# Kernel tuning notes

Hardware: AMD Instinct MI355X
Metric: run time of the kernel (lower is better)

Reference implementation:

```python
import jax, jax.numpy as jnp
import numpy as np

C_IN, C = 16, 32
N = 150000
SHAPE = (480, 360, 32)
SLOPE = 0.01  # LeakyReLU default
EPS = 1e-5    # BatchNorm1d default

# offset index into the canonical 27-neighbor table, ordered (dz, dy, dx)
P133 = tuple(9 + (dy + 1) * 3 + (dx + 1) for dy in (-1, 0, 1) for dx in (-1, 0, 1))   # kernel (1,3,3)
P313 = tuple((dz + 1) * 9 + 3 + (dx + 1) for dz in (-1, 0, 1) for dx in (-1, 0, 1))   # kernel (3,1,3)
P311 = tuple((dz + 1) * 9 + 4 for dz in (-1, 0, 1))                                   # kernel (3,1,1)
P131 = tuple(9 + (dy + 1) * 3 + 1 for dy in (-1, 0, 1))                               # kernel (1,3,1)
P113 = (12, 13, 14)                                                                   # kernel (1,1,3)


def setup_inputs() -> dict:
    rng = np.random.default_rng(0)
    # unique active voxel linear coords, sorted for searchsorted lookup
    lin = np.sort(rng.choice(SHAPE[0] * SHAPE[1] * SHAPE[2], size=N, replace=False))
    z, yx = np.divmod(lin, SHAPE[1] * SHAPE[2])
    y, x = np.divmod(yx, SHAPE[2])
    coords = np.stack([z, y, x], 1)  # [N,3]
    offs = np.array([[dz, dy, dx] for dz in (-1, 0, 1) for dy in (-1, 0, 1) for dx in (-1, 0, 1)])
    nc = coords[None] + offs[:, None]  # [27,N,3]
    valid = (nc >= 0).all(-1) & (nc[..., 0] < SHAPE[0]) & (nc[..., 1] < SHAPE[1]) & (nc[..., 2] < SHAPE[2])
    nlin = nc[..., 0] * SHAPE[1] * SHAPE[2] + nc[..., 1] * SHAPE[2] + nc[..., 2]
    pos = np.clip(np.searchsorted(lin, nlin), 0, N - 1)
    found = valid & (lin[pos] == nlin)
    nbr = np.where(found, pos, -1).astype(np.int32)  # [27,N], spconv indice pairs

    key = jax.random.key(0)
    ks = jax.random.split(key, 9)
    w = lambda k, kk, ci, co: jax.random.normal(k, (kk, ci, co), jnp.float32) * (1.0 / np.sqrt(kk * ci))
    bn_params = jnp.stack([
        jnp.stack([1.0 + 0.1 * jax.random.normal(jax.random.fold_in(ks[8], 4 * i + 0), (C,)),
                   0.1 * jax.random.normal(jax.random.fold_in(ks[8], 4 * i + 1), (C,)),
                   0.1 * jax.random.normal(jax.random.fold_in(ks[8], 4 * i + 2), (C,)),
                   0.5 + jax.random.uniform(jax.random.fold_in(ks[8], 4 * i + 3), (C,))])
        for i in range(7)
    ])  # [7,4,C]: gamma, beta, running_mean, running_var
    return {
        "x_feat": jax.random.normal(ks[0], (N, C_IN), jnp.float32),
        "nbr": jnp.asarray(nbr),
        "W1": w(ks[1], 9, C_IN, C), "W12": w(ks[2], 9, C, C),
        "W2": w(ks[3], 9, C_IN, C), "W3": w(ks[4], 9, C, C),
        "Wr1": w(ks[5], 3, C, C), "Wr2": w(ks[6], 3, C, C), "Wr3": w(ks[7], 3, C, C),
        "bn_params": bn_params,
    }


def _subm(feat, nbr, W, offs):
    """Submanifold sparse conv: gather -> masked GEMM -> same active set."""
    idx = nbr[jnp.asarray(offs)]              # [K,N]
    g = feat[jnp.clip(idx, 0)]                # [K,N,Cin]
    g = jnp.where((idx >= 0)[..., None], g, jnp.zeros((), feat.dtype))
    return jnp.einsum('knc,kcd->nd', g, W)    # [N,Cout]


def _bn(f, p):  # eval-mode BatchNorm1d
    gamma, beta, mean, var = p[0], p[1], p[2], p[3]
    return gamma * (f - mean) * jax.lax.rsqrt(var + EPS) + beta


def _lrelu(f):
    return jnp.where(f >= 0, f, SLOPE * f)


def reference(x_feat, nbr, W1, W12, W2, W3, Wr1, Wr2, Wr3, bn_params):
    # ResContextBlock (downCntx): act then BN, per source
    s = _bn(_lrelu(_subm(x_feat, nbr, W1, P133)), bn_params[0])
    s = _bn(_lrelu(_subm(s, nbr, W12, P313)), bn_params[1])
    r = _bn(_lrelu(_subm(x_feat, nbr, W2, P313)), bn_params[2])
    r = _bn(_lrelu(_subm(r, nbr, W3, P133)), bn_params[3])
    y = r + s
    # ReconBlock: three axial convs -> BN -> sigmoid, summed, gating multiply
    a = jax.nn.sigmoid(_bn(_subm(y, nbr, Wr1, P311), bn_params[4]))
    b = jax.nn.sigmoid(_bn(_subm(y, nbr, Wr2, P131), bn_params[5]))
    c = jax.nn.sigmoid(_bn(_subm(y, nbr, Wr3, P113), bn_params[6]))
    return (a + b + c) * y
```

## Files before the change

kernel.cpp:

```cpp
#include <hip/hip_runtime.h>
#include <cstdint>
#include <cstddef>


#define SLOPE 0.01f
#define BN_EPS 1e-5f

typedef __attribute__((ext_vector_type(8))) short bf16x8;
typedef __attribute__((ext_vector_type(4))) float f32x4;

__device__ __forceinline__ float bflo(uint32_t w) {
    union { uint32_t i; float f; } v; v.i = w << 16; return v.f;
}
__device__ __forceinline__ float bfhi(uint32_t w) {
    union { uint32_t i; float f; } v; v.i = w & 0xffff0000u; return v.f;
}
__device__ __forceinline__ float bf2f(uint16_t u) {
    union { uint32_t i; float f; } v; v.i = ((uint32_t)u) << 16; return v.f;
}
__device__ __forceinline__ uint16_t f2bf(float f) {
    union { float f; uint32_t i; } v; v.f = f;
    uint32_t x = v.i;
    return (uint16_t)((x + 0x7fffu + ((x >> 16) & 1u)) >> 16);
}

struct Taps9 { int t[9]; };
struct WSrcs { const void* p[8]; };

#define WFS     18432
#define WF_END  (5 * WFS)
#define BN_CNT  896

__device__ __forceinline__ int detect_f32_inline(const uint16_t* x16)
{
    int lane = threadIdx.x & 63;
    float a = bf2f(x16[4 * lane]);
    float b = bf2f(x16[4 * lane + 2]);
    int bad = (!(a > -16.f && a < 16.f)) || (!(b > -16.f && b < 16.f));
    return __ballot(bad) != 0ull;
}

__device__ __forceinline__ float readw(const void* p, int j, int f32)
{
    return f32 ? ((const float*)p)[j] : bf2f(((const uint16_t*)p)[j]);
}

__global__ void prep_all(const uint16_t* __restrict__ xprobe, WSrcs srcs,
                         uint16_t* __restrict__ Wf, float* __restrict__ bnf)
{
    int f32 = detect_f32_inline(xprobe);
    int i = blockIdx.x * 256 + threadIdx.x;
    if (i < WF_END) {
        int s = i / WFS, r = i - s * WFS;
        int t = r >> 11, T = (r >> 10) & 1;
        int co = (r >> 5) & 31, k = r & 31;
        uint16_t outv;
        if (s == 0 || s == 2) {
            int c = k >> 1, p = k & 1;
            float w = readw(srcs.p[s == 0 ? 0 : 2], (t * 16 + c) * 32 + co, f32);
            uint16_t h = f2bf(w);
            outv = (T == 0) ? h : (p == 0 ? f2bf(w - bf2f(h)) : (uint16_t)0);
        } else {
            float w;
            if (s == 4) {
                int g = t / 3, kk = t - g * 3;
                const void* bnp = srcs.p[7];
                float ga = readw(bnp, (4 + g) * 128 + co, f32);
                float va = readw(bnp, (4 + g) * 128 + 96 + co, f32);
                float scl = ga * rsqrtf(va + BN_EPS);
                w = readw(srcs.p[4 + g], (kk * 32 + k) * 32 + co, f32) * scl;
            } else {
                w = readw(srcs.p[s == 1 ? 1 : 3], (t * 32 + k) * 32 + co, f32);
            }
            uint16_t h = f2bf(w);
            outv = (T == 0) ? h : f2bf(w - bf2f(h));
        }
        Wf[i] = outv;
    } else if (i < WF_END + BN_CNT) {
        bnf[i - WF_END] = readw(srcs.p[7], i - WF_END, f32);
    }
}

__global__ void canon_x3(const void* __restrict__ xsrc,
                         uint32_t* __restrict__ xi, int total)
{
    int f32 = detect_f32_inline((const uint16_t*)xsrc);
    for (int i = blockIdx.x * blockDim.x + threadIdx.x; i < total;
         i += gridDim.x * blockDim.x) {
        float v = f32 ? ((const float*)xsrc)[i]
                      : bf2f(((const uint16_t*)xsrc)[i]);
        int row = i >> 4, c = i & 15;
        uint16_t h = f2bf(v);
        uint16_t l = f2bf(v - bf2f(h));
        xi[(size_t)row * 16 + c] = (uint32_t)h | ((uint32_t)l << 16);
    }
}

struct ConvJob {
    const uint16_t* feat;
    const uint16_t* Wf;
    const float*    bn;
    const uint16_t* addsrc;
    uint16_t*       out;
    Taps9 taps;
};

#define MFMA_BF16(A, B, C) __builtin_amdgcn_mfma_f32_16x16x32_bf16(A, B, C, 0, 0, 0)

__launch_bounds__(256, 3)
__global__ void conv_mfma5(ConvJob j0, ConvJob j1,
                           const int* __restrict__ nbr, int N)
{
    const ConvJob J = (blockIdx.y == 1) ? j1 : j0;
    const int tid = threadIdx.x;
    const int n0  = blockIdx.x * 128;
    const int lane = tid & 63;
    const int m = lane & 15, q = lane >> 4;
    const int vt0 = (tid >> 6) * 32;
    const bf16x8 Z8 = {0, 0, 0, 0, 0, 0, 0, 0};

    int rows[9][2];
#pragma unroll
    for (int t = 0; t < 9; ++t)
#pragma unroll
        for (int vt = 0; vt < 2; ++vt) {
            int n = n0 + vt0 + vt * 16 + m;
            rows[t][vt] = (n < N) ? nbr[(size_t)J.taps.t[t] * N + n] : -1;
        }
    __builtin_amdgcn_sched_barrier(0);

    bf16x8 A[9][2];
#pragma unroll
    for (int t = 0; t < 9; ++t)
#pragma unroll
        for (int vt = 0; vt < 2; ++vt) {
            int row = rows[t][vt];
            A[t][vt] = Z8;
            if (row >= 0)
                A[t][vt] = *(const bf16x8*)(J.feat + (size_t)row * 32 + q * 8);
        }
    __builtin_amdgcn_sched_barrier(0);

    f32x4 acc[2][2];
#pragma unroll
    for (int vt = 0; vt < 2; ++vt)
#pragma unroll
        for (int ot = 0; ot < 2; ++ot) acc[vt][ot] = {0.f, 0.f, 0.f, 0.f};

#pragma unroll
    for (int t = 0; t < 9; ++t) {
        const uint16_t* wb = J.Wf + t * 2048 + m * 32 + q * 8;
        bf16x8 B00 = *(const bf16x8*)(wb);
        bf16x8 B10 = *(const bf16x8*)(wb + 1024);
        bf16x8 B01 = *(const bf16x8*)(wb + 512);
        bf16x8 B11 = *(const bf16x8*)(wb + 1536);
#pragma unroll
        for (int vt = 0; vt < 2; ++vt) {
            acc[vt][0] = MFMA_BF16(A[t][vt], B00, acc[vt][0]);
            acc[vt][0] = MFMA_BF16(A[t][vt], B10, acc[vt][0]);
            acc[vt][1] = MFMA_BF16(A[t][vt], B01, acc[vt][1]);
            acc[vt][1] = MFMA_BF16(A[t][vt], B11, acc[vt][1]);
        }
    }

#pragma unroll
    for (int ot = 0; ot < 2; ++ot) {
        int ch = ot * 16 + m;
        float ga = J.bn[ch], be = J.bn[32 + ch];
        float mu = J.bn[64 + ch], va = J.bn[96 + ch];
        float s = ga * rsqrtf(va + BN_EPS);
        float b = be - mu * s;
#pragma unroll
        for (int vt = 0; vt < 2; ++vt)
#pragma unroll
            for (int r = 0; r < 4; ++r) {
                int vox = n0 + vt0 + vt * 16 + q * 4 + r;
                if (vox >= N) continue;
                float xv = acc[vt][ot][r];
                xv = (xv >= 0.f) ? xv : SLOPE * xv;
                float o = xv * s + b;
                if (J.addsrc) o += bf2f(J.addsrc[(size_t)vox * 32 + ch]);
                J.out[(size_t)vox * 32 + ch] = f2bf(o);
            }
    }
}

__launch_bounds__(256, 3)
__global__ void recon_mfma5(const uint16_t* __restrict__ y16,
                            const uint16_t* __restrict__ xprobe,
                            const int* __restrict__ nbr,
                            const uint16_t* __restrict__ Wf4,
                            const float* __restrict__ bnf,
                            void* __restrict__ out_, int N)
{
    const int out_f32 = detect_f32_inline(xprobe);
    const int tid = threadIdx.x;
    const int n0  = blockIdx.x * 128;
    const int lane = tid & 63;
    const int m = lane & 15, q = lane >> 4;
    const int vt0 = (tid >> 6) * 32;
    const bf16x8 Z8 = {0, 0, 0, 0, 0, 0, 0, 0};

    const int ut[7] = {4, 22, 10, 16, 12, 14, 13};
    int rows[7][2];
#pragma unroll
    for (int t = 0; t < 7; ++t)
#pragma unroll
        for (int vt = 0; vt < 2; ++vt) {
            int n = n0 + vt0 + vt * 16 + m;
            rows[t][vt] = (n < N) ? nbr[(size_t)ut[t] * N + n] : -1;
        }
    __builtin_amdgcn_sched_barrier(0);

    bf16x8 A[7][2];
#pragma unroll
    for (int t = 0; t < 7; ++t)
#pragma unroll
        for (int vt = 0; vt < 2; ++vt) {
            int row = rows[t][vt];
            A[t][vt] = Z8;
            if (row >= 0)
                A[t][vt] = *(const bf16x8*)(y16 + (size_t)row * 32 + q * 8);
        }
    __builtin_amdgcn_sched_barrier(0);

    f32x4 a[3][2][2];
#pragma unroll
    for (int g = 0; g < 3; ++g)
#pragma unroll
        for (int vt = 0; vt < 2; ++vt)
#pragma unroll
            for (int ot = 0; ot < 2; ++ot) a[g][vt][ot] = {0.f, 0.f, 0.f, 0.f};

#pragma unroll
    for (int e = 0; e < 3; ++e)
#pragma unroll
        for (int s2 = 0; s2 < 2; ++s2) {
            int slot = 2 * e + s2;
            int t = e * 3 + s2 * 2;
            const uint16_t* wb = Wf4 + t * 2048 + m * 32 + q * 8;
            bf16x8 B00 = *(const bf16x8*)(wb);
            bf16x8 B10 = *(const bf16x8*)(wb + 1024);
            bf16x8 B01 = *(const bf16x8*)(wb + 512);
            bf16x8 B11 = *(const bf16x8*)(wb + 1536);
#pragma unroll
            for (int vt = 0; vt < 2; ++vt) {
                a[e][vt][0] = MFMA_BF16(A[slot][vt], B00, a[e][vt][0]);
                a[e][vt][0] = MFMA_BF16(A[slot][vt], B10, a[e][vt][0]);
                a[e][vt][1] = MFMA_BF16(A[slot][vt], B01, a[e][vt][1]);
                a[e][vt][1] = MFMA_BF16(A[slot][vt], B11, a[e][vt][1]);
            }
        }
#pragma unroll
    for (int g = 0; g < 3; ++g) {
        const uint16_t* wb = Wf4 + (g * 3 + 1) * 2048 + m * 32 + q * 8;
        bf16x8 B00 = *(const bf16x8*)(wb);
        bf16x8 B10 = *(const bf16x8*)(wb + 1024);
        bf16x8 B01 = *(const bf16x8*)(wb + 512);
        bf16x8 B11 = *(const bf16x8*)(wb + 1536);
#pragma unroll
        for (int vt = 0; vt < 2; ++vt) {
            a[g][vt][0] = MFMA_BF16(A[6][vt], B00, a[g][vt][0]);
            a[g][vt][0] = MFMA_BF16(A[6][vt], B10, a[g][vt][0]);
            a[g][vt][1] = MFMA_BF16(A[6][vt], B01, a[g][vt][1]);
            a[g][vt][1] = MFMA_BF16(A[6][vt], B11, a[g][vt][1]);
        }
    }

#pragma unroll
    for (int ot = 0; ot < 2; ++ot) {
        int ch = ot * 16 + m;
        float sh[3];
#pragma unroll
        for (int g = 0; g < 3; ++g) {
            const float* p = bnf + (size_t)(4 + g) * 128;
            float scl = p[ch] * rsqrtf(p[96 + ch] + BN_EPS);
            sh[g] = p[32 + ch] - p[64 + ch] * scl;
        }
#pragma unroll
        for (int vt = 0; vt < 2; ++vt)
#pragma unroll
            for (int r = 0; r < 4; ++r) {
                int vox = n0 + vt0 + vt * 16 + q * 4 + r;
                if (vox >= N) continue;
                float g0 = 1.f / (1.f + __expf(-(a[0][vt][ot][r] + sh[0])));
                float g1 = 1.f / (1.f + __expf(-(a[1][vt][ot][r] + sh[1])));
                float g2 = 1.f / (1.f + __expf(-(a[2][vt][ot][r] + sh[2])));
                float o = (g0 + g1 + g2) * bf2f(y16[(size_t)vox * 32 + ch]);
                if (out_f32)
                    ((float*)out_)[(size_t)vox * 32 + ch] = o;
                else
                    ((uint16_t*)out_)[(size_t)vox * 32 + ch] = f2bf(o);
            }
    }
}

#define WC_W1   0
#define WC_W12  4608
#define WC_W2   13824
#define WC_W3   18432
#define WC_WR1  27648
#define WC_WR2  30720
#define WC_WR3  33792
#define WC_BNP  36864
#define WC_END  37760

__global__ void canon_weights_fb(WSrcs srcs, float* __restrict__ Wc,
                                 const uint16_t* __restrict__ xprobe)
{
    int f32 = detect_f32_inline(xprobe);
    const int offs[9] = {WC_W1, WC_W12, WC_W2, WC_W3, WC_WR1, WC_WR2,
                         WC_WR3, WC_BNP, WC_END};
    int i = blockIdx.x * 256 + threadIdx.x;
    if (i >= WC_END) return;
    int t = 0;
#pragma unroll
    for (int k = 1; k < 8; ++k) if (i >= offs[k]) t = k;
    Wc[i] = readw(srcs.p[t], i - offs[t], f32);
}

__global__ void canon_x_bf(const void* __restrict__ xsrc,
                           uint16_t* __restrict__ xc, int n)
{
    int f32 = detect_f32_inline((const uint16_t*)xsrc);
    for (int i = blockIdx.x * blockDim.x + threadIdx.x; i < n;
         i += gridDim.x * blockDim.x) {
        float v = f32 ? ((const float*)xsrc)[i]
                      : bf2f(((const uint16_t*)xsrc)[i]);
        xc[i] = f2bf(v);
    }
}

template<int CIN>
__launch_bounds__(256)
__global__ void conv_bn_lrelu_bf(const uint16_t* __restrict__ feat,
                                 const int* __restrict__ nbr,
                                 const float* __restrict__ Wg,
                                 const float* __restrict__ bnp,
                                 const uint16_t* __restrict__ addsrc,
                                 uint16_t* __restrict__ out,
                                 Taps9 taps, int N)
{
    __shared__ float Wl[9 * CIN * 32];
    __shared__ float fs[CIN][128];
    __shared__ int   sidx[128];
    __shared__ float bns[32], bnb[32];

    const int tid = threadIdx.x;
    const int n0  = blockIdx.x * 128;

    for (int i = tid; i < 9 * CIN * 32; i += 256) Wl[i] = Wg[i];
    if (tid < 32) {
        float g = bnp[tid], b = bnp[32 + tid];
        float mu = bnp[64 + tid], va = bnp[96 + tid];
        float s = g * rsqrtf(va + BN_EPS);
        bns[tid] = s; bnb[tid] = b - mu * s;
    }
    float acc[4][4];
#pragma unroll
    for (int v = 0; v < 4; ++v)
#pragma unroll
        for (int j = 0; j < 4; ++j) acc[v][j] = 0.f;

    const int vb = (tid >> 3) << 2, cg = (tid & 7) << 2;
    const int r = tid >> 1, h = tid & 1, j0 = h * (CIN / 2);

#pragma unroll 1
    for (int t = 0; t < 9; ++t) {
        __syncthreads();
        if (tid < 128) {
            int n = n0 + tid;
            sidx[tid] = (n < N) ? nbr[(size_t)taps.t[t] * N + n] : -1;
        }
        __syncthreads();
        int mm = sidx[r];
        if (mm >= 0) {
            const uint16_t* src = feat + (size_t)mm * CIN + j0;
#pragma unroll
            for (int qq = 0; qq < CIN / 2; qq += 8) {
                uint4 u = *reinterpret_cast<const uint4*>(src + qq);
                fs[j0 + qq + 0][r] = bflo(u.x); fs[j0 + qq + 1][r] = bfhi(u.x);
                fs[j0 + qq + 2][r] = bflo(u.y); fs[j0 + qq + 3][r] = bfhi(u.y);
                fs[j0 + qq + 4][r] = bflo(u.z); fs[j0 + qq + 5][r] = bfhi(u.z);
                fs[j0 + qq + 6][r] = bflo(u.w); fs[j0 + qq + 7][r] = bfhi(u.w);
            }
        } else {
#pragma unroll
            for (int qq = 0; qq < CIN / 2; ++qq) fs[j0 + qq][r] = 0.f;
        }
        __syncthreads();
        const float* wk = Wl + t * (CIN * 32) + cg;
#pragma unroll
        for (int ci = 0; ci < CIN; ++ci) {
            float4 f = *reinterpret_cast<const float4*>(&fs[ci][vb]);
            float4 w = *reinterpret_cast<const float4*>(wk + ci * 32);
            acc[0][0] += f.x * w.x; acc[0][1] += f.x * w.y; acc[0][2] += f.x * w.z; acc[0][3] += f.x * w.w;
            acc[1][0] += f.y * w.x; acc[1][1] += f.y * w.y; acc[1][2] += f.y * w.z; acc[1][3] += f.y * w.w;
            acc[2][0] += f.z * w.x; acc[2][1] += f.z * w.y; acc[2][2] += f.z * w.z; acc[2][3] += f.z * w.w;
            acc[3][0] += f.w * w.x; acc[3][1] += f.w * w.y; acc[3][2] += f.w * w.z; acc[3][3] += f.w * w.w;
        }
    }
#pragma unroll
    for (int v = 0; v < 4; ++v) {
        int n = n0 + vb + v;
        if (n >= N) continue;
        ushort4 st;
        uint16_t* ov = (uint16_t*)&st;
#pragma unroll
        for (int j = 0; j < 4; ++j) {
            float x = acc[v][j];
            x = (x >= 0.f) ? x : SLOPE * x;
            float o = x * bns[cg + j] + bnb[cg + j];
            if (addsrc) o += bf2f(addsrc[(size_t)n * 32 + cg + j]);
            ov[j] = f2bf(o);
        }
        *reinterpret_cast<ushort4*>(out + (size_t)n * 32 + cg) = st;
    }
}

__launch_bounds__(256, 4)
__global__ void recon_gate_bf(const uint16_t* __restrict__ y,
                              const int* __restrict__ nbr,
                              const float* __restrict__ Wc,
                              const uint16_t* __restrict__ xprobe,
                              void* __restrict__ out_, int N)
{
    __shared__ float Wl[3 * 32 * 32];
    __shared__ float fs[32][128];
    __shared__ int   sidx[128];
    __shared__ float scl[3][32], shf[3][32];

    const int tid = threadIdx.x;
    const int n0  = blockIdx.x * 128;
    const int out_f32 = detect_f32_inline(xprobe);

    if (tid < 96) {
        int g = tid >> 5, c = tid & 31;
        const float* p = Wc + WC_BNP + (size_t)(4 + g) * 128;
        float ga = p[c], be = p[32 + c], mu = p[64 + c], va = p[96 + c];
        float s = ga * rsqrtf(va + BN_EPS);
        scl[g][c] = s; shf[g][c] = be - mu * s;
    }
    const int vb = (tid >> 3) << 2, cg = (tid & 7) << 2;
    const int r = tid >> 1, h = tid & 1, j0 = h * 16;

    float gsum[4][4];
#pragma unroll
    for (int v = 0; v < 4; ++v)
#pragma unroll
        for (int j = 0; j < 4; ++j) gsum[v][j] = 0.f;

    const int taps[3][3] = {{4, 13, 22}, {10, 13, 16}, {12, 13, 14}};

#pragma unroll 1
    for (int g = 0; g < 3; ++g) {
        __syncthreads();
        {
            const float* src = Wc + WC_WR1 + g * 3072;
            for (int i = tid; i < 3072; i += 256)
                Wl[i] = src[i] * scl[g][i & 31];
        }
        float acc[4][4];
#pragma unroll
        for (int v = 0; v < 4; ++v)
#pragma unroll
            for (int j = 0; j < 4; ++j) acc[v][j] = 0.f;

#pragma unroll 1
        for (int k = 0; k < 3; ++k) {
            __syncthreads();
            if (tid < 128) {
                int n = n0 + tid;
                sidx[tid] = (n < N) ? nbr[(size_t)taps[g][k] * N + n] : -1;
            }
            __syncthreads();
            int mm = sidx[r];
            if (mm >= 0) {
                const uint16_t* src = y + (size_t)mm * 32 + j0;
#pragma unroll
                for (int qq = 0; qq < 16; qq += 8) {
                    uint4 u = *reinterpret_cast<const uint4*>(src + qq);
                    fs[j0 + qq + 0][r] = bflo(u.x); fs[j0 + qq + 1][r] = bfhi(u.x);
                    fs[j0 + qq + 2][r] = bflo(u.y); fs[j0 + qq + 3][r] = bfhi(u.y);
                    fs[j0 + qq + 4][r] = bflo(u.z); fs[j0 + qq + 5][r] = bfhi(u.z);
                    fs[j0 + qq + 6][r] = bflo(u.w); fs[j0 + qq + 7][r] = bfhi(u.w);
                }
            } else {
#pragma unroll
                for (int qq = 0; qq < 16; ++qq) fs[j0 + qq][r] = 0.f;
            }
            __syncthreads();
            const float* wk = Wl + k * (32 * 32) + cg;
#pragma unroll
            for (int ci = 0; ci < 32; ++ci) {
                float4 f = *reinterpret_cast<const float4*>(&fs[ci][vb]);
                float4 w = *reinterpret_cast<const float4*>(wk + ci * 32);
                acc[0][0] += f.x * w.x; acc[0][1] += f.x * w.y; acc[0][2] += f.x * w.z; acc[0][3] += f.x * w.w;
                acc[1][0] += f.y * w.x; acc[1][1] += f.y * w.y; acc[1][2] += f.y * w.z; acc[1][3] += f.y * w.w;
                acc[2][0] += f.z * w.x; acc[2][1] += f.z * w.y; acc[2][2] += f.z * w.z; acc[2][3] += f.z * w.w;
                acc[3][0] += f.w * w.x; acc[3][1] += f.w * w.y; acc[3][2] += f.w * w.z; acc[3][3] += f.w * w.w;
            }
        }
#pragma unroll
        for (int v = 0; v < 4; ++v)
#pragma unroll
            for (int j = 0; j < 4; ++j) {
                float x = acc[v][j] + shf[g][cg + j];
                gsum[v][j] += 1.f / (1.f + __expf(-x));
            }
    }
#pragma unroll
    for (int v = 0; v < 4; ++v) {
        int n = n0 + vb + v;
        if (n >= N) continue;
#pragma unroll
        for (int j = 0; j < 4; ++j) {
            float yv = bf2f(y[(size_t)n * 32 + cg + j]);
            float o = gsum[v][j] * yv;
            if (out_f32) ((float*)out_)[(size_t)n * 32 + cg + j] = o;
            else ((uint16_t*)out_)[(size_t)n * 32 + cg + j] = f2bf(o);
        }
    }
}

extern "C" void kernel_launch(void* const* d_in, const int* in_sizes, int n_in,
                              void* d_out, int out_size, void* d_ws, size_t ws_size,
                              hipStream_t stream)
{
    (void)n_in; (void)out_size;
    const void* x   = d_in[0];
    const int*  nbr = (const int*)d_in[1];
    const int N = in_sizes[0] / 16;
    const uint16_t* xprobe = (const uint16_t*)x;

    dim3 block(256);
    const int gx = (N + 127) / 128;
    Taps9 p133 = {{9, 10, 11, 12, 13, 14, 15, 16, 17}};
    Taps9 p313 = {{3, 4, 5, 12, 13, 14, 21, 22, 23}};
    WSrcs ws8 = {{ d_in[2], d_in[3], d_in[4], d_in[5],
                   d_in[6], d_in[7], d_in[8], d_in[9] }};

    float*    bnf = (float*)d_ws;
    uint16_t* Wf  = (uint16_t*)((char*)d_ws + 4096);
    const size_t base2 = 4096u + (size_t)WF_END * 2;
    uint16_t* xi  = (uint16_t*)((char*)d_ws + base2);
    uint16_t* A1  = xi + (size_t)N * 32;
    uint16_t* A2  = A1 + (size_t)N * 32;
    uint16_t* B1  = A2 + (size_t)N * 32;
    const size_t need = base2 + 4u * (size_t)N * 64;

    if (ws_size >= need) {
        prep_all<<<(WF_END + BN_CNT + 255) / 256, block, 0, stream>>>(xprobe, ws8, Wf, bnf);
        canon_x3<<<1024, block, 0, stream>>>(x, (uint32_t*)xi, N * 16);
        ConvJob c1  = {xi, Wf + 0 * WFS, bnf + 0 * 128, nullptr, A1, p133};
        ConvJob c2  = {xi, Wf + 2 * WFS, bnf + 2 * 128, nullptr, A2, p313};
        ConvJob c12 = {A1, Wf + 1 * WFS, bnf + 1 * 128, nullptr, B1, p313};
        ConvJob c3  = {A2, Wf + 3 * WFS, bnf + 3 * 128, B1,      A1, p133};
        conv_mfma5<<<dim3(gx, 2), block, 0, stream>>>(c1, c2, nbr, N);
        conv_mfma5<<<dim3(gx, 1), block, 0, stream>>>(c12, c12, nbr, N);
        conv_mfma5<<<dim3(gx, 1), block, 0, stream>>>(c3, c3, nbr, N);
        recon_mfma5<<<gx, block, 0, stream>>>(A1, xprobe, nbr, Wf + 4 * WFS, bnf, d_out, N);
    } else {
        float*    Wc = (float*)d_ws;
        uint16_t* xc = (uint16_t*)((char*)d_ws + (size_t)WC_END * 4 + 256);
        uint16_t* A  = (uint16_t*)d_out;
        uint16_t* B  = xc + (size_t)N * 16;
        const float* bn0 = Wc + WC_BNP + 0 * 128;
        const float* bn1 = Wc + WC_BNP + 1 * 128;
        const float* bn2 = Wc + WC_BNP + 2 * 128;
        const float* bn3 = Wc + WC_BNP + 3 * 128;
        canon_weights_fb<<<(WC_END + 255) / 256, block, 0, stream>>>(ws8, Wc, xprobe);
        canon_x_bf<<<1024, block, 0, stream>>>(x, xc, N * 16);
        conv_bn_lrelu_bf<16><<<gx, block, 0, stream>>>(xc, nbr, Wc + WC_W1,  bn0, nullptr, A, p133, N);
        conv_bn_lrelu_bf<32><<<gx, block, 0, stream>>>(A,  nbr, Wc + WC_W12, bn1, nullptr, B, p313, N);
        conv_bn_lrelu_bf<16><<<gx, block, 0, stream>>>(xc, nbr, Wc + WC_W2,  bn2, nullptr, A, p313, N);
        conv_bn_lrelu_bf<32><<<gx, block, 0, stream>>>(A,  nbr, Wc + WC_W3,  bn3, B,       B, p133, N);
        recon_gate_bf<<<gx, block, 0, stream>>>(B, nbr, Wc, xprobe, d_out, N);
    }
}
```

Baseline: 194.6 us.

## Gather neighbor features directly into LDS via global_load_lds with zero-row padding

Replaces register-resident gathers of neighbor feature rows with asynchronous global-to-LDS loads (global_load_lds, 16 bytes per lane). Missing neighbors point at a shared zero row written by the prep kernel. Each wave now handles 16 voxels instead of 32, halving the tiles per block and doubling the grid, which cuts VGPR pressure and should raise occupancy and latency hiding. The cost is LDS use per block and less reuse of the weight fragments per load.

```diff
diff --git a/kernel.cpp b/kernel.cpp
--- a/kernel.cpp
+++ b/kernel.cpp
@@ -30,6 +30,7 @@
 #define WFS     18432
 #define WF_END  (5 * WFS)
 #define BN_CNT  896
+#define ZROW_OFF 3584
 
 __device__ __forceinline__ int detect_f32_inline(const uint16_t* x16)
 {
@@ -43,6 +44,13 @@
 __device__ __forceinline__ float readw(const void* p, int j, int f32)
 {
     return f32 ? ((const float*)p)[j] : bf2f(((const uint16_t*)p)[j]);
+}
+
+__device__ __forceinline__ void gl_lds16(const uint16_t* g, uint16_t* l)
+{
+    __builtin_amdgcn_global_load_lds(
+        (const __attribute__((address_space(1))) uint32_t*)g,
+        (__attribute__((address_space(3))) uint32_t*)l, 16, 0, 0);
 }
 
 __global__ void prep_all(const uint16_t* __restrict__ xprobe, WSrcs srcs,
@@ -78,6 +86,8 @@
         Wf[i] = outv;
     } else if (i < WF_END + BN_CNT) {
         bnf[i - WF_END] = readw(srcs.p[7], i - WF_END, f32);
+    } else if (i < WF_END + BN_CNT + 64) {
+        ((uint16_t*)((char*)bnf + ZROW_OFF))[i - WF_END - BN_CNT] = 0;
     }
 }
 
@@ -107,60 +117,46 @@
 
 #define MFMA_BF16(A, B, C) __builtin_amdgcn_mfma_f32_16x16x32_bf16(A, B, C, 0, 0, 0)
 
-__launch_bounds__(256, 3)
-__global__ void conv_mfma5(ConvJob j0, ConvJob j1,
-                           const int* __restrict__ nbr, int N)
-{
+__launch_bounds__(256)
+__global__ void conv_mfma6(ConvJob j0, ConvJob j1,
+                           const int* __restrict__ nbr,
+                           const uint16_t* __restrict__ zrow, int N)
+{
+    __shared__ uint16_t stage[4][9][512];
     const ConvJob J = (blockIdx.y == 1) ? j1 : j0;
     const int tid = threadIdx.x;
-    const int n0  = blockIdx.x * 128;
-    const int lane = tid & 63;
+    const int w = tid >> 6, lane = tid & 63;
     const int m = lane & 15, q = lane >> 4;
-    const int vt0 = (tid >> 6) * 32;
-    const bf16x8 Z8 = {0, 0, 0, 0, 0, 0, 0, 0};
-
-    int rows[9][2];
-#pragma unroll
-    for (int t = 0; t < 9; ++t)
-#pragma unroll
-        for (int vt = 0; vt < 2; ++vt) {
-            int n = n0 + vt0 + vt * 16 + m;
-            rows[t][vt] = (n < N) ? nbr[(size_t)J.taps.t[t] * N + n] : -1;
-        }
-    __builtin_amdgcn_sched_barrier(0);
-
-    bf16x8 A[9][2];
-#pragma unroll
-    for (int t = 0; t < 9; ++t)
-#pragma unroll
-        for (int vt = 0; vt < 2; ++vt) {
-            int row = rows[t][vt];
-            A[t][vt] = Z8;
-            if (row >= 0)
-                A[t][vt] = *(const bf16x8*)(J.feat + (size_t)row * 32 + q * 8);
-        }
-    __builtin_amdgcn_sched_barrier(0);
-
-    f32x4 acc[2][2];
-#pragma unroll
-    for (int vt = 0; vt < 2; ++vt)
-#pragma unroll
-        for (int ot = 0; ot < 2; ++ot) acc[vt][ot] = {0.f, 0.f, 0.f, 0.f};
-
+    const int n0 = blockIdx.x * 64 + w * 16;
+
+    int rows[9];
 #pragma unroll
     for (int t = 0; t < 9; ++t) {
+        int n = n0 + m;
+        rows[t] = (n < N) ? nbr[(size_t)J.taps.t[t] * N + n] : -1;
+    }
+#pragma unroll
+    for (int t = 0; t < 9; ++t) {
+        const uint16_t* g = (rows[t] >= 0)
+            ? J.feat + (size_t)rows[t] * 32 + q * 8
+            : zrow + q * 8;
+        gl_lds16(g, &stage[w][t][0]);
+    }
+    asm volatile("s_waitcnt vmcnt(0)" ::: "memory");
+
+    f32x4 acc0 = {0.f, 0.f, 0.f, 0.f}, acc1 = {0.f, 0.f, 0.f, 0.f};
+#pragma unroll
+    for (int t = 0; t < 9; ++t) {
+        bf16x8 A = *(const bf16x8*)&stage[w][t][lane * 8];
         const uint16_t* wb = J.Wf + t * 2048 + m * 32 + q * 8;
         bf16x8 B00 = *(const bf16x8*)(wb);
         bf16x8 B10 = *(const bf16x8*)(wb + 1024);
         bf16x8 B01 = *(const bf16x8*)(wb + 512);
         bf16x8 B11 = *(const bf16x8*)(wb + 1536);
-#pragma unroll
-        for (int vt = 0; vt < 2; ++vt) {
-            acc[vt][0] = MFMA_BF16(A[t][vt], B00, acc[vt][0]);
-            acc[vt][0] = MFMA_BF16(A[t][vt], B10, acc[vt][0]);
-            acc[vt][1] = MFMA_BF16(A[t][vt], B01, acc[vt][1]);
-            acc[vt][1] = MFMA_BF16(A[t][vt], B11, acc[vt][1]);
-        }
+        acc0 = MFMA_BF16(A, B00, acc0);
+        acc0 = MFMA_BF16(A, B10, acc0);
+        acc1 = MFMA_BF16(A, B01, acc1);
+        acc1 = MFMA_BF16(A, B11, acc1);
     }
 
 #pragma unroll
@@ -170,67 +166,57 @@
         float mu = J.bn[64 + ch], va = J.bn[96 + ch];
         float s = ga * rsqrtf(va + BN_EPS);
         float b = be - mu * s;
-#pragma unroll
-        for (int vt = 0; vt < 2; ++vt)
-#pragma unroll
-            for (int r = 0; r < 4; ++r) {
-                int vox = n0 + vt0 + vt * 16 + q * 4 + r;
-                if (vox >= N) continue;
-                float xv = acc[vt][ot][r];
-                xv = (xv >= 0.f) ? xv : SLOPE * xv;
-                float o = xv * s + b;
-                if (J.addsrc) o += bf2f(J.addsrc[(size_t)vox * 32 + ch]);
-                J.out[(size_t)vox * 32 + ch] = f2bf(o);
-            }
-    }
-}
-
-__launch_bounds__(256, 3)
-__global__ void recon_mfma5(const uint16_t* __restrict__ y16,
+        f32x4 a = ot ? acc1 : acc0;
+#pragma unroll
+        for (int r = 0; r < 4; ++r) {
+            int vox = n0 + q * 4 + r;
+            if (vox >= N) continue;
+            float xv = a[r];
+            xv = (xv >= 0.f) ? xv : SLOPE * xv;
+            float o = xv * s + b;
+            if (J.addsrc) o += bf2f(J.addsrc[(size_t)vox * 32 + ch]);
+            J.out[(size_t)vox * 32 + ch] = f2bf(o);
+        }
+    }
+}
+
+__launch_bounds__(256)
+__global__ void recon_mfma6(const uint16_t* __restrict__ y16,
                             const uint16_t* __restrict__ xprobe,
                             const int* __restrict__ nbr,
                             const uint16_t* __restrict__ Wf4,
                             const float* __restrict__ bnf,
+                            const uint16_t* __restrict__ zrow,
                             void* __restrict__ out_, int N)
 {
+    __shared__ uint16_t stage[4][7][512];
     const int out_f32 = detect_f32_inline(xprobe);
     const int tid = threadIdx.x;
-    const int n0  = blockIdx.x * 128;
-    const int lane = tid & 63;
+    const int w = tid >> 6, lane = tid & 63;
     const int m = lane & 15, q = lane >> 4;
-    const int vt0 = (tid >> 6) * 32;
-    const bf16x8 Z8 = {0, 0, 0, 0, 0, 0, 0, 0};
+    const int n0 = blockIdx.x * 64 + w * 16;
 
     const int ut[7] = {4, 22, 10, 16, 12, 14, 13};
-    int rows[7][2];
-#pragma unroll
-    for (int t = 0; t < 7; ++t)
-#pragma unroll
-        for (int vt = 0; vt < 2; ++vt) {
-            int n = n0 + vt0 + vt * 16 + m;
-            rows[t][vt] = (n < N) ? nbr[(size_t)ut[t] * N + n] : -1;
-        }
-    __builtin_amdgcn_sched_barrier(0);
-
-    bf16x8 A[7][2];
-#pragma unroll
-    for (int t = 0; t < 7; ++t)
-#pragma unroll
-        for (int vt = 0; vt < 2; ++vt) {
-            int row = rows[t][vt];
-            A[t][vt] = Z8;
-            if (row >= 0)
-                A[t][vt] = *(const bf16x8*)(y16 + (size_t)row * 32 + q * 8);
-        }
-    __builtin_amdgcn_sched_barrier(0);
-
-    f32x4 a[3][2][2];
+    int rows[7];
+#pragma unroll
+    for (int t = 0; t < 7; ++t) {
+        int n = n0 + m;
+        rows[t] = (n < N) ? nbr[(size_t)ut[t] * N + n] : -1;
+    }
+#pragma unroll
+    for (int t = 0; t < 7; ++t) {
+        const uint16_t* g = (rows[t] >= 0)
+            ? y16 + (size_t)rows[t] * 32 + q * 8
+            : zrow + q * 8;
+        gl_lds16(g, &stage[w][t][0]);
+    }
+    asm volatile("s_waitcnt vmcnt(0)" ::: "memory");
+
+    f32x4 a[3][2];
 #pragma unroll
     for (int g = 0; g < 3; ++g)
 #pragma unroll
-        for (int vt = 0; vt < 2; ++vt)
-#pragma unroll
-            for (int ot = 0; ot < 2; ++ot) a[g][vt][ot] = {0.f, 0.f, 0.f, 0.f};
+        for (int ot = 0; ot < 2; ++ot) a[g][ot] = {0.f, 0.f, 0.f, 0.f};
 
 #pragma unroll
     for (int e = 0; e < 3; ++e)
@@ -238,32 +224,30 @@
         for (int s2 = 0; s2 < 2; ++s2) {
             int slot = 2 * e + s2;
             int t = e * 3 + s2 * 2;
+            bf16x8 A = *(const bf16x8*)&stage[w][slot][lane * 8];
             const uint16_t* wb = Wf4 + t * 2048 + m * 32 + q * 8;
             bf16x8 B00 = *(const bf16x8*)(wb);
             bf16x8 B10 = *(const bf16x8*)(wb + 1024);
             bf16x8 B01 = *(const bf16x8*)(wb + 512);
             bf16x8 B11 = *(const bf16x8*)(wb + 1536);
-#pragma unroll
-            for (int vt = 0; vt < 2; ++vt) {
-                a[e][vt][0] = MFMA_BF16(A[slot][vt], B00, a[e][vt][0]);
-                a[e][vt][0] = MFMA_BF16(A[slot][vt], B10, a[e][vt][0]);
-                a[e][vt][1] = MFMA_BF16(A[slot][vt], B01, a[e][vt][1]);
-                a[e][vt][1] = MFMA_BF16(A[slot][vt], B11, a[e][vt][1]);
-            }
-        }
-#pragma unroll
-    for (int g = 0; g < 3; ++g) {
-        const uint16_t* wb = Wf4 + (g * 3 + 1) * 2048 + m * 32 + q * 8;
-        bf16x8 B00 = *(const bf16x8*)(wb);
-        bf16x8 B10 = *(const bf16x8*)(wb + 1024);
-        bf16x8 B01 = *(const bf16x8*)(wb + 512);
-        bf16x8 B11 = *(const bf16x8*)(wb + 1536);
-#pragma unroll
-        for (int vt = 0; vt < 2; ++vt) {
-            a[g][vt][0] = MFMA_BF16(A[6][vt], B00, a[g][vt][0]);
-            a[g][vt][0] = MFMA_BF16(A[6][vt], B10, a[g][vt][0]);
-            a[g][vt][1] = MFMA_BF16(A[6][vt], B01, a[g][vt][1]);
-            a[g][vt][1] = MFMA_BF16(A[6][vt], B11, a[g][vt][1]);
+            a[e][0] = MFMA_BF16(A, B00, a[e][0]);
+            a[e][0] = MFMA_BF16(A, B10, a[e][0]);
+            a[e][1] = MFMA_BF16(A, B01, a[e][1]);
+            a[e][1] = MFMA_BF16(A, B11, a[e][1]);
+        }
+    {
+        bf16x8 A6 = *(const bf16x8*)&stage[w][6][lane * 8];
+#pragma unroll
+        for (int g = 0; g < 3; ++g) {
+            const uint16_t* wb = Wf4 + (g * 3 + 1) * 2048 + m * 32 + q * 8;
+            bf16x8 B00 = *(const bf16x8*)(wb);
+            bf16x8 B10 = *(const bf16x8*)(wb + 1024);
+            bf16x8 B01 = *(const bf16x8*)(wb + 512);
+            bf16x8 B11 = *(const bf16x8*)(wb + 1536);
+            a[g][0] = MFMA_BF16(A6, B00, a[g][0]);
+            a[g][0] = MFMA_BF16(A6, B10, a[g][0]);
+            a[g][1] = MFMA_BF16(A6, B01, a[g][1]);
+            a[g][1] = MFMA_BF16(A6, B11, a[g][1]);
         }
     }
 
@@ -278,20 +262,18 @@
             sh[g] = p[32 + ch] - p[64 + ch] * scl;
         }
 #pragma unroll
-        for (int vt = 0; vt < 2; ++vt)
-#pragma unroll
-            for (int r = 0; r < 4; ++r) {
-                int vox = n0 + vt0 + vt * 16 + q * 4 + r;
-                if (vox >= N) continue;
-                float g0 = 1.f / (1.f + __expf(-(a[0][vt][ot][r] + sh[0])));
-                float g1 = 1.f / (1.f + __expf(-(a[1][vt][ot][r] + sh[1])));
-                float g2 = 1.f / (1.f + __expf(-(a[2][vt][ot][r] + sh[2])));
-                float o = (g0 + g1 + g2) * bf2f(y16[(size_t)vox * 32 + ch]);
-                if (out_f32)
-                    ((float*)out_)[(size_t)vox * 32 + ch] = o;
-                else
-                    ((uint16_t*)out_)[(size_t)vox * 32 + ch] = f2bf(o);
-            }
+        for (int r = 0; r < 4; ++r) {
+            int vox = n0 + q * 4 + r;
+            if (vox >= N) continue;
+            float g0 = 1.f / (1.f + __expf(-(a[0][ot][r] + sh[0])));
+            float g1 = 1.f / (1.f + __expf(-(a[1][ot][r] + sh[1])));
+            float g2 = 1.f / (1.f + __expf(-(a[2][ot][r] + sh[2])));
+            float o = (g0 + g1 + g2) * bf2f(y16[(size_t)vox * 32 + ch]);
+            if (out_f32)
+                ((float*)out_)[(size_t)vox * 32 + ch] = o;
+            else
+                ((uint16_t*)out_)[(size_t)vox * 32 + ch] = f2bf(o);
+        }
     }
 }
 
@@ -534,13 +516,14 @@
     const uint16_t* xprobe = (const uint16_t*)x;
 
     dim3 block(256);
-    const int gx = (N + 127) / 128;
+    const int gx2 = (N + 63) / 64;
     Taps9 p133 = {{9, 10, 11, 12, 13, 14, 15, 16, 17}};
     Taps9 p313 = {{3, 4, 5, 12, 13, 14, 21, 22, 23}};
     WSrcs ws8 = {{ d_in[2], d_in[3], d_in[4], d_in[5],
                    d_in[6], d_in[7], d_in[8], d_in[9] }};
 
     float*    bnf = (float*)d_ws;
+    const uint16_t* zrow = (const uint16_t*)((char*)d_ws + ZROW_OFF);
     uint16_t* Wf  = (uint16_t*)((char*)d_ws + 4096);
     const size_t base2 = 4096u + (size_t)WF_END * 2;
     uint16_t* xi  = (uint16_t*)((char*)d_ws + base2);
@@ -550,16 +533,16 @@
     const size_t need = base2 + 4u * (size_t)N * 64;
 
     if (ws_size >= need) {
-        prep_all<<<(WF_END + BN_CNT + 255) / 256, block, 0, stream>>>(xprobe, ws8, Wf, bnf);
+        prep_all<<<(WF_END + BN_CNT + 64 + 255) / 256, block, 0, stream>>>(xprobe, ws8, Wf, bnf);
         canon_x3<<<1024, block, 0, stream>>>(x, (uint32_t*)xi, N * 16);
         ConvJob c1  = {xi, Wf + 0 * WFS, bnf + 0 * 128, nullptr, A1, p133};
         ConvJob c2  = {xi, Wf + 2 * WFS, bnf + 2 * 128, nullptr, A2, p313};
         ConvJob c12 = {A1, Wf + 1 * WFS, bnf + 1 * 128, nullptr, B1, p313};
         ConvJob c3  = {A2, Wf + 3 * WFS, bnf + 3 * 128, B1,      A1, p133};
-        conv_mfma5<<<dim3(gx, 2), block, 0, stream>>>(c1, c2, nbr, N);
-        conv_mfma5<<<dim3(gx, 1), block, 0, stream>>>(c12, c12, nbr, N);
-        conv_mfma5<<<dim3(gx, 1), block, 0, stream>>>(c3, c3, nbr, N);
-        recon_mfma5<<<gx, block, 0, stream>>>(A1, xprobe, nbr, Wf + 4 * WFS, bnf, d_out, N);
+        conv_mfma6<<<dim3(gx2, 2), block, 0, stream>>>(c1, c2, nbr, zrow, N);
+        conv_mfma6<<<dim3(gx2, 1), block, 0, stream>>>(c12, c12, nbr, zrow, N);
+        conv_mfma6<<<dim3(gx2, 1), block, 0, stream>>>(c3, c3, nbr, zrow, N);
+        recon_mfma6<<<gx2, block, 0, stream>>>(A1, xprobe, nbr, Wf + 4 * WFS, bnf, zrow, d_out, N);
     } else {
         float*    Wc = (float*)d_ws;
         uint16_t* xc = (uint16_t*)((char*)d_ws + (size_t)WC_END * 4 + 256);
@@ -569,6 +552,7 @@
         const float* bn1 = Wc + WC_BNP + 1 * 128;
         const float* bn2 = Wc + WC_BNP + 2 * 128;
         const float* bn3 = Wc + WC_BNP + 3 * 128;
+        const int gx = (N + 127) / 128;
         canon_weights_fb<<<(WC_END + 255) / 256, block, 0, stream>>>(ws8, Wc, xprobe);
         canon_x_bf<<<1024, block, 0, stream>>>(x, xc, N * 16);
         conv_bn_lrelu_bf<16><<<gx, block, 0, stream>>>(xc, nbr, Wc + WC_W1,  bn0, nullptr, A, p133, N);
```

Measured after the change: 246.5 us. 1.27x slower.
